# Kernel tuning notes

Measured on AMD Instinct MI355X. Metric: run time of the kernel, lower is better.

## Reference

```python
import jax, jax.numpy as jnp
import numpy as np

V, B, T, C, H, L = 32000, 4, 1024, 1024, 16, 8
HS = C // H  # head_size = 64


def _ln(x, g, b):
    m = x.mean(-1, keepdims=True)
    v = x.var(-1, keepdims=True)
    return (x - m) / jnp.sqrt(v + 1e-5) * g + b


def setup_inputs() -> dict:
    key = jax.random.key(0)
    ks = jax.random.split(key, 24)
    s = 0.02
    inp = {
        "idx": jax.random.randint(ks[0], (B, T), 0, V, dtype=jnp.int64),
        "tok_emb": jax.random.normal(ks[1], (V, C), jnp.float32) * s,
        "pos_emb": jax.random.normal(ks[2], (T, C), jnp.float32) * s,
        "Wq": jax.random.normal(ks[3], (L, H, C, HS), jnp.float32) * s,
        "Wk": jax.random.normal(ks[4], (L, H, C, HS), jnp.float32) * s,
        "Wv": jax.random.normal(ks[5], (L, H, C, HS), jnp.float32) * s,
        "Ph_w": jax.random.normal(ks[6], (L, H, HS, C), jnp.float32) * s,
        "Ph_b": jnp.zeros((L, H, C), jnp.float32),
        "Pm_w": jax.random.normal(ks[7], (L, C, C), jnp.float32) * s,
        "Pm_b": jnp.zeros((L, C), jnp.float32),
        "ln1_g": jnp.ones((L, C), jnp.float32),
        "ln1_b": jnp.zeros((L, C), jnp.float32),
        "ln2_g": jnp.ones((L, C), jnp.float32),
        "ln2_b": jnp.zeros((L, C), jnp.float32),
        "W1": jax.random.normal(ks[8], (L, C, 4 * C), jnp.float32) * s,
        "b1": jnp.zeros((L, 4 * C), jnp.float32),
        "W2": jax.random.normal(ks[9], (L, 4 * C, C), jnp.float32) * s,
        "b2": jnp.zeros((L, C), jnp.float32),
        "lnf_g": jnp.ones((C,), jnp.float32),
        "lnf_b": jnp.zeros((C,), jnp.float32),
        "head_w": jax.random.normal(ks[10], (C, V), jnp.float32) * s,
        "head_b": jnp.zeros((V,), jnp.float32),
    }
    return inp


def reference(idx, tok_emb, pos_emb, Wq, Wk, Wv, Ph_w, Ph_b, Pm_w, Pm_b,
              ln1_g, ln1_b, ln2_g, ln2_b, W1, b1, W2, b2, lnf_g, lnf_b,
              head_w, head_b):
    Bx, Tx = idx.shape
    x = tok_emb[idx] + pos_emb[:Tx]  # [B,T,C]
    mask = jnp.tril(jnp.ones((Tx, Tx), bool))
    scale = x.shape[-1] ** -0.5  # NOTE: original scales by n_embd**-0.5, not head_size
    n_layers = Wq.shape[0]
    for l in range(n_layers):
        xn = _ln(x, ln1_g[l], ln1_b[l])
        q = jnp.einsum('btc,hcs->bhts', xn, Wq[l])
        k = jnp.einsum('btc,hcs->bhts', xn, Wk[l])
        v = jnp.einsum('btc,hcs->bhts', xn, Wv[l])
        wei = jnp.einsum('bhts,bhus->bhtu', q, k) * scale
        wei = jnp.where(mask, wei, -jnp.inf)
        wei = jax.nn.softmax(wei, axis=-1)
        o = jnp.einsum('bhtu,bhus->bhts', wei, v)  # [B,H,T,HS]
        per = jnp.einsum('bhts,hsc->bhtc', o, Ph_w[l]) + Ph_b[l][None, :, None, :]
        sa = per.sum(axis=1) @ Pm_w[l] + Pm_b[l]  # combine heads, final proj
        x = x + sa
        xn2 = _ln(x, ln2_g[l], ln2_b[l])
        h = jax.nn.gelu(xn2 @ W1[l] + b1[l], approximate=False)
        x = x + h @ W2[l] + b2[l]
    x = _ln(x, lnf_g, lnf_b)
    return x @ head_w + head_b  # logits [B,T,V]
```

## Files before the change

kernel.cpp:

```cpp
#include <hip/hip_runtime.h>
#include <hip/hip_bf16.h>
#include <math.h>

static constexpr int V = 32000, B = 4, T = 1024, C = 1024, H = 16, NL = 8, HS = 64;
static constexpr int M = B * T;

typedef __bf16 bf16x8 __attribute__((ext_vector_type(8)));
typedef __bf16 bf16x4 __attribute__((ext_vector_type(4)));
typedef float f32x4 __attribute__((ext_vector_type(4)));

#define AS1 __attribute__((address_space(1)))
#define AS3 __attribute__((address_space(3)))

__global__ void k_embed(const int* __restrict__ idx, const float* __restrict__ tok,
                        const float* __restrict__ pos, float* __restrict__ x) {
  int g = blockIdx.x * blockDim.x + threadIdx.x;
  if (g >= M * C / 4) return;
  int c4 = g & 255;
  int bt = g >> 8;
  int t = bt & (T - 1);
  int row = idx[bt];
  float4 tv = *(const float4*)(tok + (size_t)row * C + c4 * 4);
  float4 pv = *(const float4*)(pos + (size_t)t * C + c4 * 4);
  float4 o;
  o.x = tv.x + pv.x; o.y = tv.y + pv.y; o.z = tv.z + pv.z; o.w = tv.w + pv.w;
  *(float4*)(x + (size_t)bt * C + c4 * 4) = o;
}

__global__ __launch_bounds__(256) void k_ln_bf(const float* __restrict__ x, const float* __restrict__ g,
                                               const float* __restrict__ b, __hip_bfloat16* __restrict__ y) {
  int row = blockIdx.x, tid = threadIdx.x;
  float4 v = ((const float4*)(x + (size_t)row * C))[tid];
  float s = v.x + v.y + v.z + v.w;
  float ss = v.x * v.x + v.y * v.y + v.z * v.z + v.w * v.w;
  for (int off = 32; off > 0; off >>= 1) {
    s += __shfl_down(s, off);
    ss += __shfl_down(ss, off);
  }
  __shared__ float sb[4], qb[4];
  int wid = tid >> 6;
  if ((tid & 63) == 0) { sb[wid] = s; qb[wid] = ss; }
  __syncthreads();
  float st = sb[0] + sb[1] + sb[2] + sb[3];
  float qt = qb[0] + qb[1] + qb[2] + qb[3];
  float mean = st * (1.0f / C);
  float var = qt * (1.0f / C) - mean * mean;
  float rstd = rsqrtf(var + 1e-5f);
  float4 gv = ((const float4*)g)[tid];
  float4 bv = ((const float4*)b)[tid];
  union { __hip_bfloat16 h[4]; ushort4 u; } pk;
  pk.h[0] = __float2bfloat16((v.x - mean) * rstd * gv.x + bv.x);
  pk.h[1] = __float2bfloat16((v.y - mean) * rstd * gv.y + bv.y);
  pk.h[2] = __float2bfloat16((v.z - mean) * rstd * gv.z + bv.z);
  pk.h[3] = __float2bfloat16((v.w - mean) * rstd * gv.w + bv.w);
  *(ushort4*)(y + (size_t)row * C + tid * 4) = pk.u;
}

__global__ __launch_bounds__(256) void k_transp(const float* __restrict__ in, __hip_bfloat16* __restrict__ out,
                                                int K, int N) {
  __shared__ float t[64][65];
  int n0 = blockIdx.x * 64, k0 = blockIdx.y * 64;
  int tx = threadIdx.x & 15, ty = threadIdx.x >> 4;
#pragma unroll
  for (int i = 0; i < 64; i += 16) {
    float4 v = *(const float4*)(in + (size_t)(k0 + ty + i) * N + n0 + tx * 4);
    t[ty + i][tx * 4 + 0] = v.x;
    t[ty + i][tx * 4 + 1] = v.y;
    t[ty + i][tx * 4 + 2] = v.z;
    t[ty + i][tx * 4 + 3] = v.w;
  }
  __syncthreads();
#pragma unroll
  for (int i = 0; i < 64; i += 16) {
    int n = ty + i;
    union { __hip_bfloat16 h[4]; ushort4 u; } pk;
#pragma unroll
    for (int j = 0; j < 4; ++j) pk.h[j] = __float2bfloat16(t[tx * 4 + j][n]);
    *(ushort4*)(out + (size_t)(n0 + n) * K + k0 + tx * 4) = pk.u;
  }
}

__global__ void k_conv(const float* __restrict__ in, __hip_bfloat16* __restrict__ out, int n4) {
  int g = blockIdx.x * blockDim.x + threadIdx.x;
  if (g >= n4) return;
  float4 v = ((const float4*)in)[g];
  union { __hip_bfloat16 h[4]; ushort4 u; } pk;
  pk.h[0] = __float2bfloat16(v.x);
  pk.h[1] = __float2bfloat16(v.y);
  pk.h[2] = __float2bfloat16(v.z);
  pk.h[3] = __float2bfloat16(v.w);
  ((ushort4*)out)[g] = pk.u;
}

__global__ __launch_bounds__(256) void k_prep_qkv(const float* __restrict__ Wq, const float* __restrict__ Wk,
                                                  const float* __restrict__ Wv, __hip_bfloat16* __restrict__ out) {
  int z = blockIdx.y;
  int sel = z >> 4, h = z & 15;
  const float* W = sel == 0 ? Wq : (sel == 1 ? Wk : Wv);
  const float* in = W + (size_t)h * C * HS;
  __hip_bfloat16* o = out + ((size_t)sel * 1024 + h * 64) * C;
  __shared__ float t[64][65];
  int k0 = blockIdx.x * 64;
  int tx = threadIdx.x & 15, ty = threadIdx.x >> 4;
#pragma unroll
  for (int i = 0; i < 64; i += 16) {
    float4 v = *(const float4*)(in + (size_t)(k0 + ty + i) * HS + tx * 4);
    t[ty + i][tx * 4 + 0] = v.x;
    t[ty + i][tx * 4 + 1] = v.y;
    t[ty + i][tx * 4 + 2] = v.z;
    t[ty + i][tx * 4 + 3] = v.w;
  }
  __syncthreads();
#pragma unroll
  for (int i = 0; i < 64; i += 16) {
    int n = ty + i;
    union { __hip_bfloat16 h4[4]; ushort4 u; } pk;
#pragma unroll
    for (int j = 0; j < 4; ++j) pk.h4[j] = __float2bfloat16(t[tx * 4 + j][n]);
    *(ushort4*)(o + (size_t)n * C + k0 + tx * 4) = pk.u;
  }
}

__global__ void k_bsum(const float* __restrict__ phb, float* __restrict__ bs) {
  int c = blockIdx.x * blockDim.x + threadIdx.x;
  if (c < C) {
    float s = 0.0f;
    for (int h = 0; h < H; ++h) s += phb[(size_t)h * C + c];
    bs[c] = s;
  }
}

__global__ void k_biascomb(const float* __restrict__ bsum, const float* __restrict__ Pm,
                           const float* __restrict__ Pmb, float* __restrict__ bc) {
  int c = blockIdx.x * blockDim.x + threadIdx.x;
  if (c < C) {
    float s = Pmb[c];
    for (int j = 0; j < C; ++j) s += bsum[j] * Pm[(size_t)j * C + c];
    bc[c] = s;
  }
}

template <int BIAS, int GELU, int RES, int OUTBF>
__global__ __launch_bounds__(256) void k_gemm_bf(const __hip_bfloat16* __restrict__ A,
                                                 const __hip_bfloat16* __restrict__ Bt,
                                                 void* Cout, const float* __restrict__ bias,
                                                 const float* res, int N, int K) {
  __shared__ __align__(16) __hip_bfloat16 As[128 * 32];
  __shared__ __align__(16) __hip_bfloat16 Bs[128 * 32];
  int bm = blockIdx.y * 128, bn = blockIdx.x * 128;
  int tid = threadIdx.x;
  int w = tid >> 6, l = tid & 63;
  int wr = (w >> 1) * 64, wc = (w & 1) * 64;
  int lr = l >> 2;
  int lk = (l & 3) * 8;
  int fr = l & 15;
  int fk = (l >> 4) * 8;
  const __hip_bfloat16* Ag = A + (size_t)bm * K;
  const __hip_bfloat16* Bg = Bt + (size_t)bn * K;
  f32x4 acc[4][4];
#pragma unroll
  for (int m = 0; m < 4; ++m)
#pragma unroll
    for (int n = 0; n < 4; ++n) acc[m][n] = (f32x4){0.f, 0.f, 0.f, 0.f};

  for (int k0 = 0; k0 < K; k0 += 32) {
    __syncthreads();
#pragma unroll
    for (int i = 0; i < 2; ++i) {
      int seg = w * 2 + i;
      int r = seg * 16 + lr;
      __builtin_amdgcn_global_load_lds((const AS1 void*)(Ag + (size_t)r * K + k0 + lk),
                                       (AS3 void*)(As + seg * 512), 16, 0, 0);
      __builtin_amdgcn_global_load_lds((const AS1 void*)(Bg + (size_t)r * K + k0 + lk),
                                       (AS3 void*)(Bs + seg * 512), 16, 0, 0);
    }
    __syncthreads();
    bf16x8 af[4], bfr[4];
#pragma unroll
    for (int m = 0; m < 4; ++m) af[m] = *(const bf16x8*)(As + ((size_t)(wr + m * 16 + fr)) * 32 + fk);
#pragma unroll
    for (int n = 0; n < 4; ++n) bfr[n] = *(const bf16x8*)(Bs + ((size_t)(wc + n * 16 + fr)) * 32 + fk);
#pragma unroll
    for (int m = 0; m < 4; ++m)
#pragma unroll
      for (int n = 0; n < 4; ++n)
        acc[m][n] = __builtin_amdgcn_mfma_f32_16x16x32_bf16(af[m], bfr[n], acc[m][n], 0, 0, 0);
  }
  int crow0 = (l >> 4) * 4;
  int ccol = l & 15;
#pragma unroll
  for (int m = 0; m < 4; ++m) {
    int row = bm + wr + m * 16 + crow0;
#pragma unroll
    for (int n = 0; n < 4; ++n) {
      int col = bn + wc + n * 16 + ccol;
      float bv = BIAS ? bias[col] : 0.0f;
#pragma unroll
      for (int r = 0; r < 4; ++r) {
        float v = acc[m][n][r] + bv;
        if (GELU) v = 0.5f * v * (1.0f + erff(v * 0.70710678118f));
        if (RES) v += res[(size_t)(row + r) * N + col];
        if (OUTBF)
          ((__hip_bfloat16*)Cout)[(size_t)(row + r) * N + col] = __float2bfloat16(v);
        else
          ((float*)Cout)[(size_t)(row + r) * N + col] = v;
      }
    }
  }
}

template <int BIAS, int GELU, int RES, int OUTBF>
__global__ __launch_bounds__(512, 2) void k_gemm256(const __hip_bfloat16* __restrict__ Ah,
                                                    const __hip_bfloat16* __restrict__ Bth,
                                                    void* Cout, const float* __restrict__ bias,
                                                    const float* res, int N, int K) {
  __shared__ __align__(16) __bf16 As[2][256 * 64];
  __shared__ __align__(16) __bf16 Bs[2][256 * 64];
  const __bf16* A = (const __bf16*)Ah;
  const __bf16* Bt = (const __bf16*)Bth;
  const int nx = N >> 8;
  const int bid = blockIdx.x;
  const int sw = ((bid & 7) * ((int)gridDim.x >> 3)) + (bid >> 3);
  const int bn = (sw % nx) << 8;
  const int bm = (sw / nx) << 8;
  const int tid = threadIdx.x, w = tid >> 6, l = tid & 63;
  const int wm = w >> 2, wn = w & 3;
  const int fr = l & 15, fg = l >> 4;
  const int srow = w * 8 + (l >> 3);
  const int scolb = ((l & 7) * 16) ^ ((l & 32) ? 32 : 0) ^ ((w & 1) ? 16 : 0);
  const __bf16* Ag = A + (size_t)(bm + srow) * K + (scolb >> 1);
  const __bf16* Bg = Bt + (size_t)(bn + srow) * K + (scolb >> 1);
  const int arow = wm * 128 + fr;
  const int brow = wn * 64 + fr;
  const int kswz = ((fr & 4) << 3) ^ ((fr & 8) << 1);

  f32x4 acc[8][4];
#pragma unroll
  for (int m = 0; m < 8; ++m)
#pragma unroll
    for (int n = 0; n < 4; ++n) acc[m][n] = (f32x4){0.f, 0.f, 0.f, 0.f};

  auto stage = [&](int bufi, size_t kel) {
    const __bf16* ag_ = Ag + kel;
    const __bf16* bg_ = Bg + kel;
#pragma unroll
    for (int jj = 0; jj < 4; ++jj)
      __builtin_amdgcn_global_load_lds((const AS1 void*)(ag_ + (size_t)jj * 64 * K),
                                       (AS3 void*)(&As[bufi][jj * 4096 + w * 512]), 16, 0, 0);
#pragma unroll
    for (int jj = 0; jj < 4; ++jj)
      __builtin_amdgcn_global_load_lds((const AS1 void*)(bg_ + (size_t)jj * 64 * K),
                                       (AS3 void*)(&Bs[bufi][jj * 4096 + w * 512]), 16, 0, 0);
  };

  const int NT = K >> 6;
  stage(0, 0);
  asm volatile("s_waitcnt vmcnt(0)" ::: "memory");
  __builtin_amdgcn_sched_barrier(0);
  __builtin_amdgcn_s_barrier();
  __builtin_amdgcn_sched_barrier(0);

  for (int t = 0; t < NT; ++t) {
    const int cb = t & 1;
    const int nb = cb ^ 1;
    bf16x8 af[4][2], bv[2][2];

#define RD_A(MG, KS) \
  (*(const bf16x8*)(&As[cb][(arow + (MG) * 16) * 64 + (((((KS) * 64) + fg * 16) ^ kswz) >> 1)]))
#define RD_B(NG, KS) \
  (*(const bf16x8*)(&Bs[cb][(brow + (NG) * 16) * 64 + (((((KS) * 64) + fg * 16) ^ kswz) >> 1)]))
#define BAR() \
  __builtin_amdgcn_sched_barrier(0); __builtin_amdgcn_s_barrier(); __builtin_amdgcn_sched_barrier(0)

#pragma unroll
    for (int m = 0; m < 4; ++m) {
      af[m][0] = RD_A(m, 0);
      af[m][1] = RD_A(m, 1);
    }
#pragma unroll
    for (int n = 0; n < 2; ++n) {
      bv[n][0] = RD_B(n, 0);
      bv[n][1] = RD_B(n, 1);
    }
    if (t + 1 < NT) stage(nb, (size_t)(t + 1) * 64);
    BAR();
    __builtin_amdgcn_s_setprio(1);
#pragma unroll
    for (int m = 0; m < 4; ++m)
#pragma unroll
      for (int n = 0; n < 2; ++n)
#pragma unroll
        for (int ks = 0; ks < 2; ++ks)
          acc[m][n] = __builtin_amdgcn_mfma_f32_16x16x32_bf16(af[m][ks], bv[n][ks], acc[m][n], 0, 0, 0);
    __builtin_amdgcn_s_setprio(0);
    BAR();

#pragma unroll
    for (int n = 0; n < 2; ++n) {
      bv[n][0] = RD_B(2 + n, 0);
      bv[n][1] = RD_B(2 + n, 1);
    }
    BAR();
    __builtin_amdgcn_s_setprio(1);
#pragma unroll
    for (int m = 0; m < 4; ++m)
#pragma unroll
      for (int n = 0; n < 2; ++n)
#pragma unroll
        for (int ks = 0; ks < 2; ++ks)
          acc[m][2 + n] = __builtin_amdgcn_mfma_f32_16x16x32_bf16(af[m][ks], bv[n][ks], acc[m][2 + n], 0, 0, 0);
    __builtin_amdgcn_s_setprio(0);
    BAR();

#pragma unroll
    for (int m = 0; m < 4; ++m) {
      af[m][0] = RD_A(4 + m, 0);
      af[m][1] = RD_A(4 + m, 1);
    }
#pragma unroll
    for (int n = 0; n < 2; ++n) {
      bv[n][0] = RD_B(n, 0);
      bv[n][1] = RD_B(n, 1);
    }
    BAR();
    __builtin_amdgcn_s_setprio(1);
#pragma unroll
    for (int m = 0; m < 4; ++m)
#pragma unroll
      for (int n = 0; n < 2; ++n)
#pragma unroll
        for (int ks = 0; ks < 2; ++ks)
          acc[4 + m][n] = __builtin_amdgcn_mfma_f32_16x16x32_bf16(af[m][ks], bv[n][ks], acc[4 + m][n], 0, 0, 0);
    __builtin_amdgcn_s_setprio(0);
    BAR();

#pragma unroll
    for (int n = 0; n < 2; ++n) {
      bv[n][0] = RD_B(2 + n, 0);
      bv[n][1] = RD_B(2 + n, 1);
    }
    BAR();
    __builtin_amdgcn_s_setprio(1);
#pragma unroll
    for (int m = 0; m < 4; ++m)
#pragma unroll
      for (int n = 0; n < 2; ++n)
#pragma unroll
        for (int ks = 0; ks < 2; ++ks)
          acc[4 + m][2 + n] = __builtin_amdgcn_mfma_f32_16x16x32_bf16(af[m][ks], bv[n][ks], acc[4 + m][2 + n], 0, 0, 0);
    __builtin_amdgcn_s_setprio(0);
    asm volatile("s_waitcnt vmcnt(0)" ::: "memory");
    BAR();
#undef RD_A
#undef RD_B
#undef BAR
  }

#pragma unroll
  for (int mg = 0; mg < 8; ++mg) {
    int row = bm + wm * 128 + mg * 16 + fg * 4;
#pragma unroll
    for (int n = 0; n < 4; ++n) {
      int col = bn + wn * 64 + n * 16 + fr;
      float bvx = BIAS ? bias[col] : 0.0f;
#pragma unroll
      for (int r = 0; r < 4; ++r) {
        float v = acc[mg][n][r] + bvx;
        if (GELU) v = 0.5f * v * (1.0f + erff(v * 0.70710678118f));
        if (RES) v += res[(size_t)(row + r) * N + col];
        if (OUTBF)
          ((__hip_bfloat16*)Cout)[(size_t)(row + r) * N + col] = __float2bfloat16(v);
        else
          ((float*)Cout)[(size_t)(row + r) * N + col] = v;
      }
    }
  }
}

__global__ __launch_bounds__(256) void k_attn(const __hip_bfloat16* __restrict__ qkvh,
                                              __hip_bfloat16* __restrict__ o) {
  const __bf16* qkv = (const __bf16*)qkvh;
  int qi = blockIdx.x;
  int bh = blockIdx.y;
  int b = bh >> 4, h = bh & 15;
  int tid = threadIdx.x;
  int w = tid >> 6, l = tid & 63;
  int fr = l & 15, fg = l >> 4;
  int qw = qi * 64 + w * 16;

  __shared__ __align__(16) __bf16 Ks[32][72];
  __shared__ __align__(16) __bf16 Vs[32][76];
  __shared__ __align__(16) __bf16 Ps[4][16][40];

  const size_t bT = (size_t)b * T;
  bf16x8 a_q[2];
  {
    const __bf16* qp = qkv + (bT + qw + fr) * 3072 + h * 64 + fg * 8;
    a_q[0] = *(const bf16x8*)qp;
    a_q[1] = *(const bf16x8*)(qp + 32);
  }
  f32x4 acc_o[4];
#pragma unroll
  for (int n = 0; n < 4; ++n) acc_o[n] = (f32x4){0.f, 0.f, 0.f, 0.f};
  float mrow[4] = {-1e30f, -1e30f, -1e30f, -1e30f};
  float lrow[4] = {0.f, 0.f, 0.f, 0.f};

  int sr = tid >> 3;
  int sc = (tid & 7) * 8;
  int ntile = (qi + 1) * 2;
  for (int t = 0; t < ntile; ++t) {
    int kv0 = t * 32;
    __syncthreads();
    {
      const __bf16* kp = qkv + (bT + kv0 + sr) * 3072 + 1024 + h * 64 + sc;
      bf16x8 k8 = *(const bf16x8*)kp;
      bf16x8 v8 = *(const bf16x8*)(kp + 1024);
      *(bf16x8*)&Ks[sr][sc] = k8;
      *(bf16x4*)&Vs[sr][sc] = __builtin_shufflevector(v8, v8, 0, 1, 2, 3);
      *(bf16x4*)&Vs[sr][sc + 4] = __builtin_shufflevector(v8, v8, 4, 5, 6, 7);
    }
    __syncthreads();
    if (kv0 > qw + 15) continue;

    f32x4 s0 = (f32x4){0.f, 0.f, 0.f, 0.f}, s1 = s0;
    s0 = __builtin_amdgcn_mfma_f32_16x16x32_bf16(a_q[0], *(const bf16x8*)&Ks[fr][fg * 8], s0, 0, 0, 0);
    s0 = __builtin_amdgcn_mfma_f32_16x16x32_bf16(a_q[1], *(const bf16x8*)&Ks[fr][32 + fg * 8], s0, 0, 0, 0);
    s1 = __builtin_amdgcn_mfma_f32_16x16x32_bf16(a_q[0], *(const bf16x8*)&Ks[16 + fr][fg * 8], s1, 0, 0, 0);
    s1 = __builtin_amdgcn_mfma_f32_16x16x32_bf16(a_q[1], *(const bf16x8*)&Ks[16 + fr][32 + fg * 8], s1, 0, 0, 0);

    int qrow = qw + fg * 4;
#pragma unroll
    for (int r = 0; r < 4; ++r) { s0[r] *= 0.03125f; s1[r] *= 0.03125f; }
    if (kv0 + 31 > qw) {
#pragma unroll
      for (int r = 0; r < 4; ++r) {
        if (kv0 + fr > qrow + r) s0[r] = -1e30f;
        if (kv0 + 16 + fr > qrow + r) s1[r] = -1e30f;
      }
    }
    float tm[4], psum[4], alpha[4];
#pragma unroll
    for (int r = 0; r < 4; ++r) tm[r] = fmaxf(s0[r], s1[r]);
#pragma unroll
    for (int off = 1; off < 16; off <<= 1)
#pragma unroll
      for (int r = 0; r < 4; ++r) tm[r] = fmaxf(tm[r], __shfl_xor(tm[r], off));
#pragma unroll
    for (int r = 0; r < 4; ++r) {
      float mnew = fmaxf(mrow[r], tm[r]);
      alpha[r] = __expf(mrow[r] - mnew);
      mrow[r] = mnew;
      float p0 = __expf(s0[r] - mnew);
      float p1 = __expf(s1[r] - mnew);
      s0[r] = p0; s1[r] = p1;
      psum[r] = p0 + p1;
    }
#pragma unroll
    for (int off = 1; off < 16; off <<= 1)
#pragma unroll
      for (int r = 0; r < 4; ++r) psum[r] += __shfl_xor(psum[r], off);
#pragma unroll
    for (int r = 0; r < 4; ++r) lrow[r] = lrow[r] * alpha[r] + psum[r];
#pragma unroll
    for (int n = 0; n < 4; ++n)
#pragma unroll
      for (int r = 0; r < 4; ++r) acc_o[n][r] *= alpha[r];

#pragma unroll
    for (int r = 0; r < 4; ++r) {
      Ps[w][fg * 4 + r][fr] = (__bf16)s0[r];
      Ps[w][fg * 4 + r][16 + fr] = (__bf16)s1[r];
    }
    bf16x8 a_p = *(const bf16x8*)&Ps[w][fr][fg * 8];
#pragma unroll
    for (int n = 0; n < 4; ++n) {
      bf16x8 bvv;
#pragma unroll
      for (int j = 0; j < 8; ++j) bvv[j] = Vs[fg * 8 + j][n * 16 + fr];
      acc_o[n] = __builtin_amdgcn_mfma_f32_16x16x32_bf16(a_p, bvv, acc_o[n], 0, 0, 0);
    }
  }
  float inv[4];
#pragma unroll
  for (int r = 0; r < 4; ++r) inv[r] = 1.0f / lrow[r];
  __bf16* ob = (__bf16*)o;
#pragma unroll
  for (int n = 0; n < 4; ++n)
#pragma unroll
    for (int r = 0; r < 4; ++r)
      ob[(bT + qw + fg * 4 + r) * 1024 + h * 64 + n * 16 + fr] = (__bf16)(acc_o[n][r] * inv[r]);
}

extern "C" void kernel_launch(void* const* d_in, const int* in_sizes, int n_in,
                              void* d_out, int out_size, void* d_ws, size_t ws_size,
                              hipStream_t stream) {
  const int* idx = (const int*)d_in[0];
  const float* tok = (const float*)d_in[1];
  const float* pos = (const float*)d_in[2];
  const float* Wq = (const float*)d_in[3];
  const float* Wk = (const float*)d_in[4];
  const float* Wv = (const float*)d_in[5];
  const float* Phw = (const float*)d_in[6];
  const float* Phb = (const float*)d_in[7];
  const float* Pmw = (const float*)d_in[8];
  const float* Pmb = (const float*)d_in[9];
  const float* ln1g = (const float*)d_in[10];
  const float* ln1b = (const float*)d_in[11];
  const float* ln2g = (const float*)d_in[12];
  const float* ln2b = (const float*)d_in[13];
  const float* W1 = (const float*)d_in[14];
  const float* b1 = (const float*)d_in[15];
  const float* W2 = (const float*)d_in[16];
  const float* b2 = (const float*)d_in[17];
  const float* lnfg = (const float*)d_in[18];
  const float* lnfb = (const float*)d_in[19];
  const float* headw = (const float*)d_in[20];
  const float* headb = (const float*)d_in[21];
  float* out = (float*)d_out;

  char* p = (char*)d_ws;
  float* x = (float*)p;                       p += (size_t)M * C * 4;
  float* bsumv = (float*)p;                   p += 4096;
  float* bcv = (float*)p;                     p += 4096;
  char* layer_region = p;
  __hip_bfloat16* qkvb = (__hip_bfloat16*)p;  p += (size_t)M * 3072 * 2;
  __hip_bfloat16* ob = (__hip_bfloat16*)p;    p += (size_t)M * C * 2;
  __hip_bfloat16* hb = (__hip_bfloat16*)p;    p += (size_t)M * 4 * C * 2;
  __hip_bfloat16* wt = (__hip_bfloat16*)p;    p += (size_t)4 * C * C * 2;
  __hip_bfloat16* wtPmT = (__hip_bfloat16*)p; p += (size_t)C * C * 2;
  __hip_bfloat16* wtPh = (__hip_bfloat16*)p;  p += (size_t)C * C * 2;
  __hip_bfloat16* wcombT = (__hip_bfloat16*)p; p += (size_t)C * C * 2;
  __hip_bfloat16* xn = (__hip_bfloat16*)p;    p += (size_t)M * C * 2;
  __hip_bfloat16* wt_head = (__hip_bfloat16*)layer_region;

  k_embed<<<(M * C / 4 + 255) / 256, 256, 0, stream>>>(idx, tok, pos, x);

  for (int l = 0; l < NL; ++l) {
    k_ln_bf<<<M, 256, 0, stream>>>(x, ln1g + (size_t)l * C, ln1b + (size_t)l * C, xn);
    k_prep_qkv<<<dim3(16, 48), 256, 0, stream>>>(Wq + (size_t)l * H * C * HS, Wk + (size_t)l * H * C * HS,
                                                 Wv + (size_t)l * H * C * HS, wt);
    k_gemm256<0, 0, 0, 1><<<(3072 / 256) * (M / 256), 512, 0, stream>>>(xn, wt, qkvb, nullptr, nullptr, 3072, C);
    k_attn<<<dim3(T / 64, B * H), 256, 0, stream>>>(qkvb, ob);
    k_bsum<<<(C + 255) / 256, 256, 0, stream>>>(Phb + (size_t)l * H * C, bsumv);
    k_transp<<<dim3(16, 16), 256, 0, stream>>>(Pmw + (size_t)l * C * C, wtPmT, C, C);
    k_conv<<<(C * C / 4 + 255) / 256, 256, 0, stream>>>(Phw + (size_t)l * H * HS * C, wtPh, C * C / 4);
    k_gemm_bf<0, 0, 0, 1><<<dim3(C / 128, C / 128), 256, 0, stream>>>(wtPmT, wtPh, wcombT, nullptr, nullptr, C, C);
    k_biascomb<<<(C + 255) / 256, 256, 0, stream>>>(bsumv, Pmw + (size_t)l * C * C, Pmb + (size_t)l * C, bcv);
    k_gemm_bf<1, 0, 1, 0><<<dim3(C / 128, M / 128), 256, 0, stream>>>(ob, wcombT, x, bcv, x, C, C);
    k_ln_bf<<<M, 256, 0, stream>>>(x, ln2g + (size_t)l * C, ln2b + (size_t)l * C, xn);
    k_transp<<<dim3(64, 16), 256, 0, stream>>>(W1 + (size_t)l * C * 4 * C, wt, C, 4 * C);
    k_gemm256<1, 1, 0, 1><<<(4 * C / 256) * (M / 256), 512, 0, stream>>>(xn, wt, hb, b1 + (size_t)l * 4 * C, nullptr, 4 * C, C);
    k_transp<<<dim3(16, 64), 256, 0, stream>>>(W2 + (size_t)l * 4 * C * C, wt, 4 * C, C);
    k_gemm_bf<1, 0, 1, 0><<<dim3(C / 128, M / 128), 256, 0, stream>>>(hb, wt, x, b2 + (size_t)l * C, x, C, 4 * C);
  }

  k_ln_bf<<<M, 256, 0, stream>>>(x, lnfg, lnfb, xn);
  k_transp<<<dim3(500, 16), 256, 0, stream>>>(headw, wt_head, C, V);
  k_gemm256<1, 0, 0, 0><<<(V / 256) * (M / 256), 512, 0, stream>>>(xn, wt_head, out, headb, nullptr, V, C);
}
```

Measured before the change: 4.211 ms.

## Keep all B fragments in registers and rework LDS swizzle in 256 GEMM

The 256x256 GEMM main loop now holds all four B fragment groups in registers, so the second half of the M tile reuses them instead of reading B from LDS again. This removes two LDS read phases and two barrier pairs per K step. The shared-memory XOR swizzle for both the global-to-LDS staging and the fragment reads is replaced with a new pattern meant to cut LDS bank conflicts. The cost is higher VGPR pressure under launch_bounds(512,2), which could cause spills or lower occupancy.

```diff
diff --git a/kernel.cpp b/kernel.cpp
--- a/kernel.cpp
+++ b/kernel.cpp
@@ -227,12 +227,12 @@
   const int wm = w >> 2, wn = w & 3;
   const int fr = l & 15, fg = l >> 4;
   const int srow = w * 8 + (l >> 3);
-  const int scolb = ((l & 7) * 16) ^ ((l & 32) ? 32 : 0) ^ ((w & 1) ? 16 : 0);
+  const int scolb = ((l & 7) << 4) ^ ((l & 8) << 3) ^ ((l & 16) << 1) ^ ((l & 32) >> 1);
   const __bf16* Ag = A + (size_t)(bm + srow) * K + (scolb >> 1);
   const __bf16* Bg = Bt + (size_t)(bn + srow) * K + (scolb >> 1);
   const int arow = wm * 128 + fr;
   const int brow = wn * 64 + fr;
-  const int kswz = ((fr & 4) << 3) ^ ((fr & 8) << 1);
+  const int kswz = ((fr & 1) << 6) | ((fr & 2) << 4) | ((fr & 4) << 2);
 
   f32x4 acc[8][4];
 #pragma unroll
@@ -263,12 +263,12 @@
   for (int t = 0; t < NT; ++t) {
     const int cb = t & 1;
     const int nb = cb ^ 1;
-    bf16x8 af[4][2], bv[2][2];
+    bf16x8 af[4][2], bv[4][2];
 
 #define RD_A(MG, KS) \
-  (*(const bf16x8*)(&As[cb][(arow + (MG) * 16) * 64 + (((((KS) * 64) + fg * 16) ^ kswz) >> 1)]))
+  (*(const bf16x8*)(&As[cb][(arow + (MG) * 16) * 64 + ((((KS) * 64 + fg * 16) ^ kswz) >> 1)]))
 #define RD_B(NG, KS) \
-  (*(const bf16x8*)(&Bs[cb][(brow + (NG) * 16) * 64 + (((((KS) * 64) + fg * 16) ^ kswz) >> 1)]))
+  (*(const bf16x8*)(&Bs[cb][(brow + (NG) * 16) * 64 + ((((KS) * 64 + fg * 16) ^ kswz) >> 1)]))
 #define BAR() \
   __builtin_amdgcn_sched_barrier(0); __builtin_amdgcn_s_barrier(); __builtin_amdgcn_sched_barrier(0)
 
@@ -297,8 +297,8 @@
 
 #pragma unroll
     for (int n = 0; n < 2; ++n) {
-      bv[n][0] = RD_B(2 + n, 0);
-      bv[n][1] = RD_B(2 + n, 1);
+      bv[2 + n][0] = RD_B(2 + n, 0);
+      bv[2 + n][1] = RD_B(2 + n, 1);
     }
     BAR();
     __builtin_amdgcn_s_setprio(1);
@@ -308,7 +308,7 @@
       for (int n = 0; n < 2; ++n)
 #pragma unroll
         for (int ks = 0; ks < 2; ++ks)
-          acc[m][2 + n] = __builtin_amdgcn_mfma_f32_16x16x32_bf16(af[m][ks], bv[n][ks], acc[m][2 + n], 0, 0, 0);
+          acc[m][2 + n] = __builtin_amdgcn_mfma_f32_16x16x32_bf16(af[m][ks], bv[2 + n][ks], acc[m][2 + n], 0, 0, 0);
     __builtin_amdgcn_s_setprio(0);
     BAR();
 
@@ -317,37 +317,15 @@
       af[m][0] = RD_A(4 + m, 0);
       af[m][1] = RD_A(4 + m, 1);
     }
-#pragma unroll
-    for (int n = 0; n < 2; ++n) {
-      bv[n][0] = RD_B(n, 0);
-      bv[n][1] = RD_B(n, 1);
-    }
     BAR();
     __builtin_amdgcn_s_setprio(1);
 #pragma unroll
     for (int m = 0; m < 4; ++m)
 #pragma unroll
-      for (int n = 0; n < 2; ++n)
+      for (int n = 0; n < 4; ++n)
 #pragma unroll
         for (int ks = 0; ks < 2; ++ks)
           acc[4 + m][n] = __builtin_amdgcn_mfma_f32_16x16x32_bf16(af[m][ks], bv[n][ks], acc[4 + m][n], 0, 0, 0);
-    __builtin_amdgcn_s_setprio(0);
-    BAR();
-
-#pragma unroll
-    for (int n = 0; n < 2; ++n) {
-      bv[n][0] = RD_B(2 + n, 0);
-      bv[n][1] = RD_B(2 + n, 1);
-    }
-    BAR();
-    __builtin_amdgcn_s_setprio(1);
-#pragma unroll
-    for (int m = 0; m < 4; ++m)
-#pragma unroll
-      for (int n = 0; n < 2; ++n)
-#pragma unroll
-        for (int ks = 0; ks < 2; ++ks)
-          acc[4 + m][2 + n] = __builtin_amdgcn_mfma_f32_16x16x32_bf16(af[m][ks], bv[n][ks], acc[4 + m][2 + n], 0, 0, 0);
     __builtin_amdgcn_s_setprio(0);
     asm volatile("s_waitcnt vmcnt(0)" ::: "memory");
     BAR();
```

New measurement: 3.967 ms. 5.8% less time.
